# Performance work log

Hardware: AMD Instinct MI355X
Metric: run time of the kernel (lower is better)

Reference implementation:

```python
import jax, jax.numpy as jnp
import numpy as np

B, Hh, Ww, C, D = 32, 14, 14, 512, 8192

def setup_inputs() -> dict:
    key = jax.random.key(0)
    k1, k2, k3, k4, k5, k6 = jax.random.split(key, 6)
    bottom1 = jax.random.normal(k1, (B, Hh, Ww, C), dtype=jnp.float32)
    bottom2 = jax.random.normal(k2, (B, Hh, Ww, C), dtype=jnp.float32)
    # rand_s: random +/-1 (trainable weights in the original layer)
    rand_s_1 = (2.0 * jax.random.randint(k3, (C,), 0, 2).astype(jnp.float32) - 1.0)
    rand_s_2 = (2.0 * jax.random.randint(k4, (C,), 0, 2).astype(jnp.float32) - 1.0)
    # rand_h: hash bucket index in [0, D) per input channel (fixed, non-trainable)
    rand_h_1 = jax.random.randint(k5, (C,), 0, D, dtype=jnp.int32)
    rand_h_2 = jax.random.randint(k6, (C,), 0, D, dtype=jnp.int32)
    return {"bottom1": bottom1, "bottom2": bottom2,
            "rand_s_1": rand_s_1, "rand_s_2": rand_s_2,
            "rand_h_1": rand_h_1, "rand_h_2": rand_h_2}

def _count_sketch(x_flat, rand_s, rand_h, out_dim):
    # x_flat: [N, C]. Equivalent to x_flat @ sparse_sketch_matrix [C, out_dim]
    # where sketch[c, rand_h[c]] = rand_s[c].
    z = x_flat * rand_s                                   # [N, C]
    # scatter-add channels into their hash buckets along the feature axis
    return jax.ops.segment_sum(z.T, rand_h, num_segments=out_dim).T  # [N, D]

def reference(bottom1, bottom2, rand_s_1, rand_s_2, rand_h_1, rand_h_2):
    b, h, w, c1 = bottom1.shape
    c2 = bottom2.shape[-1]
    x1 = bottom1.reshape(-1, c1)
    x2 = bottom2.reshape(-1, c2)
    sk1 = _count_sketch(x1, rand_s_1, rand_h_1, D)        # [N, D]
    sk2 = _count_sketch(x2, rand_s_2, rand_h_2, D)        # [N, D]
    fft1 = jnp.fft.fft(sk1.astype(jnp.complex64), axis=-1)
    fft2 = jnp.fft.fft(sk2.astype(jnp.complex64), axis=-1)
    cbp_flat = jnp.real(jnp.fft.ifft(fft1 * fft2, axis=-1))  # circular conv
    cbp = cbp_flat.reshape(b, h, w, D)
    return jnp.sum(cbp, axis=(1, 2))                      # [B, D]
```

## Files before the change

kernel.cpp:

```cpp
#include <hip/hip_runtime.h>


#define NB   32
#define HW   196
#define CC   512
#define DD   8192
#define KP   224
#define NTHR 256
#define TILES_PER_B 16

typedef __attribute__((ext_vector_type(8)))  __bf16 bf8;
typedef __attribute__((ext_vector_type(16))) float  f32x16;

#define XT_ELEMS ((size_t)NB * CC * KP)
#define XT_BYTES (XT_ELEMS * 2)
#define PART_OFF_BYTES (2 * XT_BYTES)
#define PART_BYTES ((size_t)NB * TILES_PER_B * DD * 4)
#define NEED_FAST (PART_OFF_BYTES + PART_BYTES)
#define NEED_R5  PART_BYTES

__global__ __launch_bounds__(NTHR) void cbp_transpose_kernel(
    const float* __restrict__ x1, const float* __restrict__ x2,
    __bf16* __restrict__ xT1, __bf16* __restrict__ xT2)
{
    __shared__ float T[64][65];
    const int bid = blockIdx.x;
    const int b  = bid >> 5;
    const int ct = (bid >> 2) & 7;
    const int kt = bid & 3;
    const int tid = threadIdx.x;

    #pragma unroll
    for (int m = 0; m < 2; ++m) {
        const float* x   = m ? x2  : x1;
        __bf16*      xTo = m ? xT2 : xT1;

        #pragma unroll
        for (int p = 0; p < 4; ++p) {
            const int row  = p * 16 + (tid >> 4);
            const int col4 = (tid & 15) * 4;
            const int k = kt * 64 + row;
            float4 v = {0.f, 0.f, 0.f, 0.f};
            if (k < HW)
                v = *(const float4*)(x + ((size_t)(b * HW + k) * CC + ct * 64 + col4));
            T[col4 + 0][row] = v.x;
            T[col4 + 1][row] = v.y;
            T[col4 + 2][row] = v.z;
            T[col4 + 3][row] = v.w;
        }
        __syncthreads();

        const int c_l = tid >> 2;
        const int seg = tid & 3;
        const int kp0 = kt * 64 + seg * 16;
        if (kp0 < KP) {
            const size_t dstc = (size_t)(b * CC + ct * 64 + c_l) * KP;
            #pragma unroll
            for (int i2 = 0; i2 < 2; ++i2) {
                bf8 v;
                #pragma unroll
                for (int i = 0; i < 8; ++i)
                    v[i] = (__bf16)T[c_l][seg * 16 + i2 * 8 + i];
                *(bf8*)(xTo + dstc + kp0 + i2 * 8) = v;
            }
        }
        __syncthreads();
    }
}

__global__ __launch_bounds__(NTHR) void cbp_gram_t_kernel(
    const __bf16* __restrict__ xT1, const __bf16* __restrict__ xT2,
    const float* __restrict__ s1, const float* __restrict__ s2,
    const int*   __restrict__ h1, const int*   __restrict__ h2,
    float* __restrict__ partials)
{
    __shared__ float accD[DD];

    const int bid  = blockIdx.x;
    const int b    = bid >> 4;
    const int t1   = (bid >> 2) & 3;
    const int t2   = bid & 3;
    const int tid  = threadIdx.x;
    const int wid  = tid >> 6;
    const int lane = tid & 63;
    const int wr   = wid >> 1;
    const int wc   = wid & 1;
    const int lo5  = lane & 31;
    const int hi   = lane >> 5;

    for (int i = tid; i < DD; i += NTHR) accD[i] = 0.0f;
    __syncthreads();

    const int c1w = t1 * 128 + wr * 64;
    const int c2w = t2 * 128 + wc * 64;

    const __bf16* A0 = xT1 + ((size_t)(b * CC + c1w + lo5) * KP + hi * 8);
    const __bf16* A1 = A0 + (size_t)32 * KP;
    const __bf16* B0 = xT2 + ((size_t)(b * CC + c2w + lo5) * KP + hi * 8);
    const __bf16* B1 = B0 + (size_t)32 * KP;

    f32x16 acc00 = {}, acc01 = {}, acc10 = {}, acc11 = {};

    #pragma unroll
    for (int ks = 0; ks < KP / 16; ++ks) {
        const bf8 a0  = *(const bf8*)(A0 + ks * 16);
        const bf8 a1  = *(const bf8*)(A1 + ks * 16);
        const bf8 b0v = *(const bf8*)(B0 + ks * 16);
        const bf8 b1v = *(const bf8*)(B1 + ks * 16);
        acc00 = __builtin_amdgcn_mfma_f32_32x32x16_bf16(a0, b0v, acc00, 0, 0, 0);
        acc01 = __builtin_amdgcn_mfma_f32_32x32x16_bf16(a0, b1v, acc01, 0, 0, 0);
        acc10 = __builtin_amdgcn_mfma_f32_32x32x16_bf16(a1, b0v, acc10, 0, 0, 0);
        acc11 = __builtin_amdgcn_mfma_f32_32x32x16_bf16(a1, b1v, acc11, 0, 0, 0);
    }

    const float s2v0 = s2[c2w + lo5];
    const float s2v1 = s2[c2w + 32 + lo5];
    const int   h2v0 = h2[c2w + lo5];
    const int   h2v1 = h2[c2w + 32 + lo5];

    #pragma unroll
    for (int rt = 0; rt < 2; ++rt) {
        const f32x16 accL = rt ? acc10 : acc00;
        const f32x16 accR = rt ? acc11 : acc01;
        #pragma unroll
        for (int reg = 0; reg < 16; ++reg) {
            const int c1 = c1w + rt * 32 + (reg & 3) + 8 * (reg >> 2) + 4 * hi;
            const float sv = s1[c1];
            const int   hv = h1[c1];
            atomicAdd(&accD[(hv + h2v0) & (DD - 1)], sv * s2v0 * accL[reg]);
            atomicAdd(&accD[(hv + h2v1) & (DD - 1)], sv * s2v1 * accR[reg]);
        }
    }
    __syncthreads();

    float4* dst = (float4*)(partials + (size_t)bid * DD);
    const float4* src = (const float4*)accD;
    #pragma unroll
    for (int i = 0; i < DD / 4 / NTHR; ++i)
        dst[tid + i * NTHR] = src[tid + i * NTHR];
}

__global__ __launch_bounds__(NTHR) void cbp_mfma_kernel(
    const float* __restrict__ x1, const float* __restrict__ x2,
    const float* __restrict__ s1, const float* __restrict__ s2,
    const int*   __restrict__ h1, const int*   __restrict__ h2,
    float* __restrict__ ws, float* __restrict__ out, int use_ws)
{
    __shared__ float accD[DD];
    const int bid  = blockIdx.x;
    const int b    = bid >> 4;
    const int t1   = (bid >> 2) & 3;
    const int t2   = bid & 3;
    const int tid  = threadIdx.x;
    const int wid  = tid >> 6;
    const int lane = tid & 63;
    const int wr   = wid >> 1;
    const int wc   = wid & 1;
    const int lo5  = lane & 31;
    const int hi   = lane >> 5;

    for (int i = tid; i < DD; i += NTHR) accD[i] = 0.0f;
    __syncthreads();

    const int c1w = t1 * 128 + wr * 64;
    const int c2w = t2 * 128 + wc * 64;
    const float* A0 = x1 + (size_t)b * HW * CC + (c1w + lo5);
    const float* A1 = A0 + 32;
    const float* B0 = x2 + (size_t)b * HW * CC + (c2w + lo5);
    const float* B1 = B0 + 32;

    f32x16 acc00 = {}, acc01 = {}, acc10 = {}, acc11 = {};
    for (int ks = 0; ks < 12; ++ks) {
        const int kb = ks * 16 + hi * 8;
        bf8 a0, a1, b0v, b1v;
        #pragma unroll
        for (int j = 0; j < 8; ++j) {
            const size_t off = (size_t)(kb + j) * CC;
            a0[j] = (__bf16)A0[off]; a1[j] = (__bf16)A1[off];
            b0v[j] = (__bf16)B0[off]; b1v[j] = (__bf16)B1[off];
        }
        acc00 = __builtin_amdgcn_mfma_f32_32x32x16_bf16(a0, b0v, acc00, 0, 0, 0);
        acc01 = __builtin_amdgcn_mfma_f32_32x32x16_bf16(a0, b1v, acc01, 0, 0, 0);
        acc10 = __builtin_amdgcn_mfma_f32_32x32x16_bf16(a1, b0v, acc10, 0, 0, 0);
        acc11 = __builtin_amdgcn_mfma_f32_32x32x16_bf16(a1, b1v, acc11, 0, 0, 0);
    }
    {
        const int kb = 192 + hi * 8;
        bf8 a0, a1, b0v, b1v;
        #pragma unroll
        for (int j = 0; j < 8; ++j) {
            const int k = kb + j;
            const size_t off = (size_t)k * CC;
            const bool v = (k < HW);
            a0[j]  = (__bf16)(v ? A0[off] : 0.0f);
            a1[j]  = (__bf16)(v ? A1[off] : 0.0f);
            b0v[j] = (__bf16)(v ? B0[off] : 0.0f);
            b1v[j] = (__bf16)(v ? B1[off] : 0.0f);
        }
        acc00 = __builtin_amdgcn_mfma_f32_32x32x16_bf16(a0, b0v, acc00, 0, 0, 0);
        acc01 = __builtin_amdgcn_mfma_f32_32x32x16_bf16(a0, b1v, acc01, 0, 0, 0);
        acc10 = __builtin_amdgcn_mfma_f32_32x32x16_bf16(a1, b0v, acc10, 0, 0, 0);
        acc11 = __builtin_amdgcn_mfma_f32_32x32x16_bf16(a1, b1v, acc11, 0, 0, 0);
    }

    const float s2v0 = s2[c2w + lo5];
    const float s2v1 = s2[c2w + 32 + lo5];
    const int   h2v0 = h2[c2w + lo5];
    const int   h2v1 = h2[c2w + 32 + lo5];
    #pragma unroll
    for (int rt = 0; rt < 2; ++rt) {
        const f32x16 accL = rt ? acc10 : acc00;
        const f32x16 accR = rt ? acc11 : acc01;
        #pragma unroll
        for (int reg = 0; reg < 16; ++reg) {
            const int c1 = c1w + rt * 32 + (reg & 3) + 8 * (reg >> 2) + 4 * hi;
            const float sv = s1[c1];
            const int   hv = h1[c1];
            atomicAdd(&accD[(hv + h2v0) & (DD - 1)], sv * s2v0 * accL[reg]);
            atomicAdd(&accD[(hv + h2v1) & (DD - 1)], sv * s2v1 * accR[reg]);
        }
    }
    __syncthreads();

    if (use_ws) {
        float4* dst = (float4*)(ws + (size_t)bid * DD);
        const float4* src = (const float4*)accD;
        #pragma unroll
        for (int i = 0; i < DD / 4 / NTHR; ++i)
            dst[tid + i * NTHR] = src[tid + i * NTHR];
    } else {
        float* ob = out + (size_t)b * DD;
        for (int i = tid; i < DD; i += NTHR)
            atomicAdd(&ob[i], accD[i]);
    }
}

__global__ __launch_bounds__(NTHR) void cbp_reduce_kernel(
    const float* __restrict__ parts, float* __restrict__ out)
{
    const int b  = blockIdx.x >> 3;
    const int d0 = (blockIdx.x & 7) * 1024 + threadIdx.x * 4;
    const float* base = parts + (size_t)b * TILES_PER_B * DD + d0;
    float4 sum = {0.f, 0.f, 0.f, 0.f};
    #pragma unroll
    for (int t = 0; t < TILES_PER_B; ++t) {
        float4 v = *(const float4*)(base + (size_t)t * DD);
        sum.x += v.x; sum.y += v.y; sum.z += v.z; sum.w += v.w;
    }
    *(float4*)(out + (size_t)b * DD + d0) = sum;
}

extern "C" void kernel_launch(void* const* d_in, const int* in_sizes, int n_in,
                              void* d_out, int out_size, void* d_ws, size_t ws_size,
                              hipStream_t stream) {
    const float* x1 = (const float*)d_in[0];
    const float* x2 = (const float*)d_in[1];
    const float* s1 = (const float*)d_in[2];
    const float* s2 = (const float*)d_in[3];
    const int*   h1 = (const int*)d_in[4];
    const int*   h2 = (const int*)d_in[5];
    float* out = (float*)d_out;

    dim3 block(NTHR);
    if (ws_size >= NEED_FAST) {
        __bf16* xT1 = (__bf16*)d_ws;
        __bf16* xT2 = xT1 + XT_ELEMS;
        float*  parts = (float*)((char*)d_ws + PART_OFF_BYTES);
        cbp_transpose_kernel<<<dim3(NB * 32), block, 0, stream>>>(x1, x2, xT1, xT2);
        cbp_gram_t_kernel<<<dim3(NB * TILES_PER_B), block, 0, stream>>>(
            xT1, xT2, s1, s2, h1, h2, parts);
        cbp_reduce_kernel<<<dim3(NB * 8), block, 0, stream>>>(parts, out);
    } else if (ws_size >= NEED_R5) {
        float* parts = (float*)d_ws;
        cbp_mfma_kernel<<<dim3(NB * TILES_PER_B), block, 0, stream>>>(
            x1, x2, s1, s2, h1, h2, parts, out, 1);
        cbp_reduce_kernel<<<dim3(NB * 8), block, 0, stream>>>(parts, out);
    } else {
        hipMemsetAsync(out, 0, (size_t)out_size * sizeof(float), stream);
        cbp_mfma_kernel<<<dim3(NB * TILES_PER_B), block, 0, stream>>>(
            x1, x2, s1, s2, h1, h2, (float*)d_ws, out, 0);
    }
}
```

Measured before the change: 143.1 us.

## Split gram and hash-scatter into separate kernels, drop transpose pass

```diff
diff --git a/kernel.cpp b/kernel.cpp
--- a/kernel.cpp
+++ b/kernel.cpp
@@ -5,77 +5,22 @@
 #define HW   196
 #define CC   512
 #define DD   8192
-#define KP   224
 #define NTHR 256
 #define TILES_PER_B 16
 
 typedef __attribute__((ext_vector_type(8)))  __bf16 bf8;
 typedef __attribute__((ext_vector_type(16))) float  f32x16;
 
-#define XT_ELEMS ((size_t)NB * CC * KP)
-#define XT_BYTES (XT_ELEMS * 2)
-#define PART_OFF_BYTES (2 * XT_BYTES)
+#define G_BYTES   ((size_t)NB * TILES_PER_B * 128 * 128 * 4)
 #define PART_BYTES ((size_t)NB * TILES_PER_B * DD * 4)
-#define NEED_FAST (PART_OFF_BYTES + PART_BYTES)
-#define NEED_R5  PART_BYTES
-
-__global__ __launch_bounds__(NTHR) void cbp_transpose_kernel(
+#define NEED_SPLIT (G_BYTES + PART_BYTES)
+#define NEED_R5   PART_BYTES
+
+__global__ __launch_bounds__(NTHR) void cbp_gram_store_kernel(
     const float* __restrict__ x1, const float* __restrict__ x2,
-    __bf16* __restrict__ xT1, __bf16* __restrict__ xT2)
-{
-    __shared__ float T[64][65];
-    const int bid = blockIdx.x;
-    const int b  = bid >> 5;
-    const int ct = (bid >> 2) & 7;
-    const int kt = bid & 3;
-    const int tid = threadIdx.x;
-
-    #pragma unroll
-    for (int m = 0; m < 2; ++m) {
-        const float* x   = m ? x2  : x1;
-        __bf16*      xTo = m ? xT2 : xT1;
-
-        #pragma unroll
-        for (int p = 0; p < 4; ++p) {
-            const int row  = p * 16 + (tid >> 4);
-            const int col4 = (tid & 15) * 4;
-            const int k = kt * 64 + row;
-            float4 v = {0.f, 0.f, 0.f, 0.f};
-            if (k < HW)
-                v = *(const float4*)(x + ((size_t)(b * HW + k) * CC + ct * 64 + col4));
-            T[col4 + 0][row] = v.x;
-            T[col4 + 1][row] = v.y;
-            T[col4 + 2][row] = v.z;
-            T[col4 + 3][row] = v.w;
-        }
-        __syncthreads();
-
-        const int c_l = tid >> 2;
-        const int seg = tid & 3;
-        const int kp0 = kt * 64 + seg * 16;
-        if (kp0 < KP) {
-            const size_t dstc = (size_t)(b * CC + ct * 64 + c_l) * KP;
-            #pragma unroll
-            for (int i2 = 0; i2 < 2; ++i2) {
-                bf8 v;
-                #pragma unroll
-                for (int i = 0; i < 8; ++i)
-                    v[i] = (__bf16)T[c_l][seg * 16 + i2 * 8 + i];
-                *(bf8*)(xTo + dstc + kp0 + i2 * 8) = v;
-            }
-        }
-        __syncthreads();
-    }
-}
-
-__global__ __launch_bounds__(NTHR) void cbp_gram_t_kernel(
-    const __bf16* __restrict__ xT1, const __bf16* __restrict__ xT2,
     const float* __restrict__ s1, const float* __restrict__ s2,
-    const int*   __restrict__ h1, const int*   __restrict__ h2,
-    float* __restrict__ partials)
-{
-    __shared__ float accD[DD];
-
+    float* __restrict__ G)
+{
     const int bid  = blockIdx.x;
     const int b    = bid >> 4;
     const int t1   = (bid >> 2) & 3;
@@ -88,48 +33,99 @@
     const int lo5  = lane & 31;
     const int hi   = lane >> 5;
 
-    for (int i = tid; i < DD; i += NTHR) accD[i] = 0.0f;
-    __syncthreads();
-
     const int c1w = t1 * 128 + wr * 64;
     const int c2w = t2 * 128 + wc * 64;
 
-    const __bf16* A0 = xT1 + ((size_t)(b * CC + c1w + lo5) * KP + hi * 8);
-    const __bf16* A1 = A0 + (size_t)32 * KP;
-    const __bf16* B0 = xT2 + ((size_t)(b * CC + c2w + lo5) * KP + hi * 8);
-    const __bf16* B1 = B0 + (size_t)32 * KP;
+    const float* A0 = x1 + (size_t)b * HW * CC + (c1w + lo5);
+    const float* A1 = A0 + 32;
+    const float* B0 = x2 + (size_t)b * HW * CC + (c2w + lo5);
+    const float* B1 = B0 + 32;
+
+    const float sA0 = s1[c1w + lo5],      sA1 = s1[c1w + 32 + lo5];
+    const float sB0 = s2[c2w + lo5],      sB1 = s2[c2w + 32 + lo5];
 
     f32x16 acc00 = {}, acc01 = {}, acc10 = {}, acc11 = {};
 
-    #pragma unroll
-    for (int ks = 0; ks < KP / 16; ++ks) {
-        const bf8 a0  = *(const bf8*)(A0 + ks * 16);
-        const bf8 a1  = *(const bf8*)(A1 + ks * 16);
-        const bf8 b0v = *(const bf8*)(B0 + ks * 16);
-        const bf8 b1v = *(const bf8*)(B1 + ks * 16);
-        acc00 = __builtin_amdgcn_mfma_f32_32x32x16_bf16(a0, b0v, acc00, 0, 0, 0);
-        acc01 = __builtin_amdgcn_mfma_f32_32x32x16_bf16(a0, b1v, acc01, 0, 0, 0);
-        acc10 = __builtin_amdgcn_mfma_f32_32x32x16_bf16(a1, b0v, acc10, 0, 0, 0);
-        acc11 = __builtin_amdgcn_mfma_f32_32x32x16_bf16(a1, b1v, acc11, 0, 0, 0);
-    }
-
-    const float s2v0 = s2[c2w + lo5];
-    const float s2v1 = s2[c2w + 32 + lo5];
-    const int   h2v0 = h2[c2w + lo5];
-    const int   h2v1 = h2[c2w + 32 + lo5];
-
+    for (int ks = 0; ks < 12; ++ks) {
+        const int kb = ks * 16 + hi * 8;
+        bf8 a0, a1, b0v, b1v;
+        #pragma unroll
+        for (int j = 0; j < 8; ++j) {
+            const size_t off = (size_t)(kb + j) * CC;
+            a0[j]  = (__bf16)(A0[off] * sA0);
+            a1[j]  = (__bf16)(A1[off] * sA1);
+            b0v[j] = (__bf16)(B0[off] * sB0);
+            b1v[j] = (__bf16)(B1[off] * sB1);
+        }
+        acc00 = __builtin_amdgcn_mfma_f32_32x32x16_bf16(a0, b0v, acc00, 0, 0, 0);
+        acc01 = __builtin_amdgcn_mfma_f32_32x32x16_bf16(a0, b1v, acc01, 0, 0, 0);
+        acc10 = __builtin_amdgcn_mfma_f32_32x32x16_bf16(a1, b0v, acc10, 0, 0, 0);
+        acc11 = __builtin_amdgcn_mfma_f32_32x32x16_bf16(a1, b1v, acc11, 0, 0, 0);
+    }
+    {
+        const int kb = 192 + hi * 8;
+        bf8 a0, a1, b0v, b1v;
+        #pragma unroll
+        for (int j = 0; j < 8; ++j) {
+            const int k = kb + j;
+            const size_t off = (size_t)k * CC;
+            const bool v = (k < HW);
+            a0[j]  = (__bf16)(v ? A0[off] * sA0 : 0.0f);
+            a1[j]  = (__bf16)(v ? A1[off] * sA1 : 0.0f);
+            b0v[j] = (__bf16)(v ? B0[off] * sB0 : 0.0f);
+            b1v[j] = (__bf16)(v ? B1[off] * sB1 : 0.0f);
+        }
+        acc00 = __builtin_amdgcn_mfma_f32_32x32x16_bf16(a0, b0v, acc00, 0, 0, 0);
+        acc01 = __builtin_amdgcn_mfma_f32_32x32x16_bf16(a0, b1v, acc01, 0, 0, 0);
+        acc10 = __builtin_amdgcn_mfma_f32_32x32x16_bf16(a1, b0v, acc10, 0, 0, 0);
+        acc11 = __builtin_amdgcn_mfma_f32_32x32x16_bf16(a1, b1v, acc11, 0, 0, 0);
+    }
+
+    float* Gt = G + (size_t)bid * (128 * 128);
     #pragma unroll
     for (int rt = 0; rt < 2; ++rt) {
         const f32x16 accL = rt ? acc10 : acc00;
         const f32x16 accR = rt ? acc11 : acc01;
         #pragma unroll
         for (int reg = 0; reg < 16; ++reg) {
-            const int c1 = c1w + rt * 32 + (reg & 3) + 8 * (reg >> 2) + 4 * hi;
-            const float sv = s1[c1];
-            const int   hv = h1[c1];
-            atomicAdd(&accD[(hv + h2v0) & (DD - 1)], sv * s2v0 * accL[reg]);
-            atomicAdd(&accD[(hv + h2v1) & (DD - 1)], sv * s2v1 * accR[reg]);
-        }
+            const int c1l = wr * 64 + rt * 32 + (reg & 3) + 8 * (reg >> 2) + 4 * hi;
+            Gt[c1l * 128 + wc * 64 + lo5]      = accL[reg];
+            Gt[c1l * 128 + wc * 64 + 32 + lo5] = accR[reg];
+        }
+    }
+}
+
+__global__ __launch_bounds__(NTHR) void cbp_scatter_kernel(
+    const float* __restrict__ G,
+    const int* __restrict__ h1, const int* __restrict__ h2,
+    float* __restrict__ partials)
+{
+    __shared__ float accD[DD];
+    __shared__ int   h1t[128];
+    __shared__ int   h2t[128];
+
+    const int bid = blockIdx.x;
+    const int t1  = (bid >> 2) & 3;
+    const int t2  = bid & 3;
+    const int tid = threadIdx.x;
+
+    if (tid < 128)      h1t[tid]       = h1[t1 * 128 + tid];
+    else if (tid < 256) h2t[tid - 128] = h2[t2 * 128 + (tid - 128)];
+    for (int i = tid; i < DD; i += NTHR) accD[i] = 0.0f;
+    __syncthreads();
+
+    const float4* Gt = (const float4*)(G + (size_t)bid * (128 * 128));
+    #pragma unroll
+    for (int i = 0; i < 16; ++i) {
+        const int idx  = tid + i * NTHR;
+        const int c1l  = idx >> 5;
+        const int c2l4 = (idx & 31) * 4;
+        const float4 v = Gt[idx];
+        const int hb = h1t[c1l];
+        unsafeAtomicAdd(&accD[(hb + h2t[c2l4 + 0]) & (DD - 1)], v.x);
+        unsafeAtomicAdd(&accD[(hb + h2t[c2l4 + 1]) & (DD - 1)], v.y);
+        unsafeAtomicAdd(&accD[(hb + h2t[c2l4 + 2]) & (DD - 1)], v.z);
+        unsafeAtomicAdd(&accD[(hb + h2t[c2l4 + 3]) & (DD - 1)], v.w);
     }
     __syncthreads();
 
@@ -138,6 +134,21 @@
     #pragma unroll
     for (int i = 0; i < DD / 4 / NTHR; ++i)
         dst[tid + i * NTHR] = src[tid + i * NTHR];
+}
+
+__global__ __launch_bounds__(NTHR) void cbp_reduce_kernel(
+    const float* __restrict__ parts, float* __restrict__ out)
+{
+    const int b  = blockIdx.x >> 3;
+    const int d0 = (blockIdx.x & 7) * 1024 + threadIdx.x * 4;
+    const float* base = parts + (size_t)b * TILES_PER_B * DD + d0;
+    float4 sum = {0.f, 0.f, 0.f, 0.f};
+    #pragma unroll
+    for (int t = 0; t < TILES_PER_B; ++t) {
+        float4 v = *(const float4*)(base + (size_t)t * DD);
+        sum.x += v.x; sum.y += v.y; sum.z += v.z; sum.w += v.w;
+    }
+    *(float4*)(out + (size_t)b * DD + d0) = sum;
 }
 
 __global__ __launch_bounds__(NTHR) void cbp_mfma_kernel(
@@ -216,8 +227,8 @@
             const int c1 = c1w + rt * 32 + (reg & 3) + 8 * (reg >> 2) + 4 * hi;
             const float sv = s1[c1];
             const int   hv = h1[c1];
-            atomicAdd(&accD[(hv + h2v0) & (DD - 1)], sv * s2v0 * accL[reg]);
-            atomicAdd(&accD[(hv + h2v1) & (DD - 1)], sv * s2v1 * accR[reg]);
+            unsafeAtomicAdd(&accD[(hv + h2v0) & (DD - 1)], sv * s2v0 * accL[reg]);
+            unsafeAtomicAdd(&accD[(hv + h2v1) & (DD - 1)], sv * s2v1 * accR[reg]);
         }
     }
     __syncthreads();
@@ -233,21 +244,6 @@
         for (int i = tid; i < DD; i += NTHR)
             atomicAdd(&ob[i], accD[i]);
     }
-}
-
-__global__ __launch_bounds__(NTHR) void cbp_reduce_kernel(
-    const float* __restrict__ parts, float* __restrict__ out)
-{
-    const int b  = blockIdx.x >> 3;
-    const int d0 = (blockIdx.x & 7) * 1024 + threadIdx.x * 4;
-    const float* base = parts + (size_t)b * TILES_PER_B * DD + d0;
-    float4 sum = {0.f, 0.f, 0.f, 0.f};
-    #pragma unroll
-    for (int t = 0; t < TILES_PER_B; ++t) {
-        float4 v = *(const float4*)(base + (size_t)t * DD);
-        sum.x += v.x; sum.y += v.y; sum.z += v.z; sum.w += v.w;
-    }
-    *(float4*)(out + (size_t)b * DD + d0) = sum;
 }
 
 extern "C" void kernel_launch(void* const* d_in, const int* in_sizes, int n_in,
@@ -262,13 +258,13 @@
     float* out = (float*)d_out;
 
     dim3 block(NTHR);
-    if (ws_size >= NEED_FAST) {
-        __bf16* xT1 = (__bf16*)d_ws;
-        __bf16* xT2 = xT1 + XT_ELEMS;
-        float*  parts = (float*)((char*)d_ws + PART_OFF_BYTES);
-        cbp_transpose_kernel<<<dim3(NB * 32), block, 0, stream>>>(x1, x2, xT1, xT2);
-        cbp_gram_t_kernel<<<dim3(NB * TILES_PER_B), block, 0, stream>>>(
-            xT1, xT2, s1, s2, h1, h2, parts);
+    if (ws_size >= NEED_SPLIT) {
+        float* G     = (float*)d_ws;
+        float* parts = (float*)((char*)d_ws + G_BYTES);
+        cbp_gram_store_kernel<<<dim3(NB * TILES_PER_B), block, 0, stream>>>(
+            x1, x2, s1, s2, G);
+        cbp_scatter_kernel<<<dim3(NB * TILES_PER_B), block, 0, stream>>>(
+            G, h1, h2, parts);
         cbp_reduce_kernel<<<dim3(NB * 8), block, 0, stream>>>(parts, out);
     } else if (ws_size >= NEED_R5) {
         float* parts = (float*)d_ws;
```

Measured after the change: 178.7 us. 1.25x slower.

## Split Gram GEMM from hash scatter into separate kernels with sign folding

Applied to the files above, without the earlier changes.

```diff
diff --git a/kernel.cpp b/kernel.cpp
--- a/kernel.cpp
+++ b/kernel.cpp
@@ -12,15 +12,16 @@
 typedef __attribute__((ext_vector_type(8)))  __bf16 bf8;
 typedef __attribute__((ext_vector_type(16))) float  f32x16;
 
-#define XT_ELEMS ((size_t)NB * CC * KP)
-#define XT_BYTES (XT_ELEMS * 2)
-#define PART_OFF_BYTES (2 * XT_BYTES)
+#define G_BYTES    ((size_t)NB * TILES_PER_B * 128 * 128 * 4)
+#define XT_ELEMS   ((size_t)NB * CC * KP)
+#define XT_BYTES   (XT_ELEMS * 2)
 #define PART_BYTES ((size_t)NB * TILES_PER_B * DD * 4)
-#define NEED_FAST (PART_OFF_BYTES + PART_BYTES)
-#define NEED_R5  PART_BYTES
+#define NEED_SPLIT (G_BYTES + PART_BYTES)
+#define NEED_R5    PART_BYTES
 
 __global__ __launch_bounds__(NTHR) void cbp_transpose_kernel(
     const float* __restrict__ x1, const float* __restrict__ x2,
+    const float* __restrict__ s1, const float* __restrict__ s2,
     __bf16* __restrict__ xT1, __bf16* __restrict__ xT2)
 {
     __shared__ float T[64][65];
@@ -33,6 +34,7 @@
     #pragma unroll
     for (int m = 0; m < 2; ++m) {
         const float* x   = m ? x2  : x1;
+        const float* s   = m ? s2  : s1;
         __bf16*      xTo = m ? xT2 : xT1;
 
         #pragma unroll
@@ -54,13 +56,14 @@
         const int seg = tid & 3;
         const int kp0 = kt * 64 + seg * 16;
         if (kp0 < KP) {
+            const float sv = s[ct * 64 + c_l];
             const size_t dstc = (size_t)(b * CC + ct * 64 + c_l) * KP;
             #pragma unroll
             for (int i2 = 0; i2 < 2; ++i2) {
                 bf8 v;
                 #pragma unroll
                 for (int i = 0; i < 8; ++i)
-                    v[i] = (__bf16)T[c_l][seg * 16 + i2 * 8 + i];
+                    v[i] = (__bf16)(T[c_l][seg * 16 + i2 * 8 + i] * sv);
                 *(bf8*)(xTo + dstc + kp0 + i2 * 8) = v;
             }
         }
@@ -68,68 +71,88 @@
     }
 }
 
-__global__ __launch_bounds__(NTHR) void cbp_gram_t_kernel(
+__global__ __launch_bounds__(NTHR, 5) void cbp_gram2_kernel(
     const __bf16* __restrict__ xT1, const __bf16* __restrict__ xT2,
-    const float* __restrict__ s1, const float* __restrict__ s2,
-    const int*   __restrict__ h1, const int*   __restrict__ h2,
-    float* __restrict__ partials)
-{
-    __shared__ float accD[DD];
-
+    float* __restrict__ G)
+{
     const int bid  = blockIdx.x;
-    const int b    = bid >> 4;
-    const int t1   = (bid >> 2) & 3;
-    const int t2   = bid & 3;
+    const int swz  = (bid & 7) * 256 + (bid >> 3);
     const int tid  = threadIdx.x;
     const int wid  = tid >> 6;
     const int lane = tid & 63;
-    const int wr   = wid >> 1;
-    const int wc   = wid & 1;
     const int lo5  = lane & 31;
     const int hi   = lane >> 5;
 
+    const int t  = swz * 4 + wid;
+    const int b  = t >> 8;
+    const int r  = t & 255;
+    const int u1 = r >> 4;
+    const int u2 = r & 15;
+
+    const __bf16* A  = xT1 + ((size_t)(b * CC + u1 * 32 + lo5) * KP + hi * 8);
+    const __bf16* Bp = xT2 + ((size_t)(b * CC + u2 * 32 + lo5) * KP + hi * 8);
+
+    f32x16 acc = {};
+    bf8 Af[7], Bf[7];
+
+    #pragma unroll
+    for (int s = 0; s < 7; ++s) {
+        Af[s] = *(const bf8*)(A  + s * 16);
+        Bf[s] = *(const bf8*)(Bp + s * 16);
+    }
+    #pragma unroll
+    for (int s = 0; s < 7; ++s)
+        acc = __builtin_amdgcn_mfma_f32_32x32x16_bf16(Af[s], Bf[s], acc, 0, 0, 0);
+
+    #pragma unroll
+    for (int s = 0; s < 7; ++s) {
+        Af[s] = *(const bf8*)(A  + (7 + s) * 16);
+        Bf[s] = *(const bf8*)(Bp + (7 + s) * 16);
+    }
+    #pragma unroll
+    for (int s = 0; s < 7; ++s)
+        acc = __builtin_amdgcn_mfma_f32_32x32x16_bf16(Af[s], Bf[s], acc, 0, 0, 0);
+
+    float* Gt = G + (size_t)(b * 16 + (u1 >> 2) * 4 + (u2 >> 2)) * (128 * 128);
+    const int c2l = (u2 & 3) * 32 + lo5;
+    #pragma unroll
+    for (int reg = 0; reg < 16; ++reg) {
+        const int c1l = (u1 & 3) * 32 + (reg & 3) + 8 * (reg >> 2) + 4 * hi;
+        Gt[c1l * 128 + c2l] = acc[reg];
+    }
+}
+
+__global__ __launch_bounds__(NTHR) void cbp_scatter_kernel(
+    const float* __restrict__ G,
+    const int* __restrict__ h1, const int* __restrict__ h2,
+    float* __restrict__ partials)
+{
+    __shared__ float accD[DD];
+    __shared__ int   h1t[128];
+    __shared__ int   h2t[128];
+
+    const int bid = blockIdx.x;
+    const int t1  = (bid >> 2) & 3;
+    const int t2  = bid & 3;
+    const int tid = threadIdx.x;
+
+    if (tid < 128)      h1t[tid]       = h1[t1 * 128 + tid];
+    else if (tid < 256) h2t[tid - 128] = h2[t2 * 128 + (tid - 128)];
     for (int i = tid; i < DD; i += NTHR) accD[i] = 0.0f;
     __syncthreads();
 
-    const int c1w = t1 * 128 + wr * 64;
-    const int c2w = t2 * 128 + wc * 64;
-
-    const __bf16* A0 = xT1 + ((size_t)(b * CC + c1w + lo5) * KP + hi * 8);
-    const __bf16* A1 = A0 + (size_t)32 * KP;
-    const __bf16* B0 = xT2 + ((size_t)(b * CC + c2w + lo5) * KP + hi * 8);
-    const __bf16* B1 = B0 + (size_t)32 * KP;
-
-    f32x16 acc00 = {}, acc01 = {}, acc10 = {}, acc11 = {};
-
-    #pragma unroll
-    for (int ks = 0; ks < KP / 16; ++ks) {
-        const bf8 a0  = *(const bf8*)(A0 + ks * 16);
-        const bf8 a1  = *(const bf8*)(A1 + ks * 16);
-        const bf8 b0v = *(const bf8*)(B0 + ks * 16);
-        const bf8 b1v = *(const bf8*)(B1 + ks * 16);
-        acc00 = __builtin_amdgcn_mfma_f32_32x32x16_bf16(a0, b0v, acc00, 0, 0, 0);
-        acc01 = __builtin_amdgcn_mfma_f32_32x32x16_bf16(a0, b1v, acc01, 0, 0, 0);
-        acc10 = __builtin_amdgcn_mfma_f32_32x32x16_bf16(a1, b0v, acc10, 0, 0, 0);
-        acc11 = __builtin_amdgcn_mfma_f32_32x32x16_bf16(a1, b1v, acc11, 0, 0, 0);
-    }
-
-    const float s2v0 = s2[c2w + lo5];
-    const float s2v1 = s2[c2w + 32 + lo5];
-    const int   h2v0 = h2[c2w + lo5];
-    const int   h2v1 = h2[c2w + 32 + lo5];
-
-    #pragma unroll
-    for (int rt = 0; rt < 2; ++rt) {
-        const f32x16 accL = rt ? acc10 : acc00;
-        const f32x16 accR = rt ? acc11 : acc01;
-        #pragma unroll
-        for (int reg = 0; reg < 16; ++reg) {
-            const int c1 = c1w + rt * 32 + (reg & 3) + 8 * (reg >> 2) + 4 * hi;
-            const float sv = s1[c1];
-            const int   hv = h1[c1];
-            atomicAdd(&accD[(hv + h2v0) & (DD - 1)], sv * s2v0 * accL[reg]);
-            atomicAdd(&accD[(hv + h2v1) & (DD - 1)], sv * s2v1 * accR[reg]);
-        }
+    const float4* Gt = (const float4*)(G + (size_t)bid * (128 * 128));
+    #pragma unroll
+    for (int i = 0; i < 16; ++i) {
+        const int idx  = tid + i * NTHR;
+        const int c1l  = idx >> 5;
+        const int c2l4 = (idx & 31) * 4;
+        const float4 v = Gt[idx];
+        const int hb = h1t[c1l];
+        unsafeAtomicAdd(&accD[(hb + h2t[c2l4 + 0]) & (DD - 1)], v.x);
+        unsafeAtomicAdd(&accD[(hb + h2t[c2l4 + 1]) & (DD - 1)], v.y);
+        unsafeAtomicAdd(&accD[(hb + h2t[c2l4 + 2]) & (DD - 1)], v.z);
+        unsafeAtomicAdd(&accD[(hb + h2t[c2l4 + 3]) & (DD - 1)], v.w);
     }
     __syncthreads();
 
@@ -138,6 +161,21 @@
     #pragma unroll
     for (int i = 0; i < DD / 4 / NTHR; ++i)
         dst[tid + i * NTHR] = src[tid + i * NTHR];
+}
+
+__global__ __launch_bounds__(NTHR) void cbp_reduce_kernel(
+    const float* __restrict__ parts, float* __restrict__ out)
+{
+    const int b  = blockIdx.x >> 3;
+    const int d0 = (blockIdx.x & 7) * 1024 + threadIdx.x * 4;
+    const float* base = parts + (size_t)b * TILES_PER_B * DD + d0;
+    float4 sum = {0.f, 0.f, 0.f, 0.f};
+    #pragma unroll
+    for (int t = 0; t < TILES_PER_B; ++t) {
+        float4 v = *(const float4*)(base + (size_t)t * DD);
+        sum.x += v.x; sum.y += v.y; sum.z += v.z; sum.w += v.w;
+    }
+    *(float4*)(out + (size_t)b * DD + d0) = sum;
 }
 
 __global__ __launch_bounds__(NTHR) void cbp_mfma_kernel(
@@ -216,8 +254,8 @@
             const int c1 = c1w + rt * 32 + (reg & 3) + 8 * (reg >> 2) + 4 * hi;
             const float sv = s1[c1];
             const int   hv = h1[c1];
-            atomicAdd(&accD[(hv + h2v0) & (DD - 1)], sv * s2v0 * accL[reg]);
-            atomicAdd(&accD[(hv + h2v1) & (DD - 1)], sv * s2v1 * accR[reg]);
+            unsafeAtomicAdd(&accD[(hv + h2v0) & (DD - 1)], sv * s2v0 * accL[reg]);
+            unsafeAtomicAdd(&accD[(hv + h2v1) & (DD - 1)], sv * s2v1 * accR[reg]);
         }
     }
     __syncthreads();
@@ -233,21 +271,6 @@
         for (int i = tid; i < DD; i += NTHR)
             atomicAdd(&ob[i], accD[i]);
     }
-}
-
-__global__ __launch_bounds__(NTHR) void cbp_reduce_kernel(
-    const float* __restrict__ parts, float* __restrict__ out)
-{
-    const int b  = blockIdx.x >> 3;
-    const int d0 = (blockIdx.x & 7) * 1024 + threadIdx.x * 4;
-    const float* base = parts + (size_t)b * TILES_PER_B * DD + d0;
-    float4 sum = {0.f, 0.f, 0.f, 0.f};
-    #pragma unroll
-    for (int t = 0; t < TILES_PER_B; ++t) {
-        float4 v = *(const float4*)(base + (size_t)t * DD);
-        sum.x += v.x; sum.y += v.y; sum.z += v.z; sum.w += v.w;
-    }
-    *(float4*)(out + (size_t)b * DD + d0) = sum;
 }
 
 extern "C" void kernel_launch(void* const* d_in, const int* in_sizes, int n_in,
@@ -262,13 +285,16 @@
     float* out = (float*)d_out;
 
     dim3 block(NTHR);
-    if (ws_size >= NEED_FAST) {
-        __bf16* xT1 = (__bf16*)d_ws;
-        __bf16* xT2 = xT1 + XT_ELEMS;
-        float*  parts = (float*)((char*)d_ws + PART_OFF_BYTES);
-        cbp_transpose_kernel<<<dim3(NB * 32), block, 0, stream>>>(x1, x2, xT1, xT2);
-        cbp_gram_t_kernel<<<dim3(NB * TILES_PER_B), block, 0, stream>>>(
-            xT1, xT2, s1, s2, h1, h2, parts);
+    if (ws_size >= NEED_SPLIT) {
+        float*  G     = (float*)d_ws;
+        __bf16* xT1   = (__bf16*)((char*)d_ws + G_BYTES);
+        __bf16* xT2   = xT1 + XT_ELEMS;
+        float*  parts = (float*)((char*)d_ws + G_BYTES);
+        cbp_transpose_kernel<<<dim3(NB * 32), block, 0, stream>>>(
+            x1, x2, s1, s2, xT1, xT2);
+        cbp_gram2_kernel<<<dim3(2048), block, 0, stream>>>(xT1, xT2, G);
+        cbp_scatter_kernel<<<dim3(NB * TILES_PER_B), block, 0, stream>>>(
+            G, h1, h2, parts);
         cbp_reduce_kernel<<<dim3(NB * 8), block, 0, stream>>>(parts, out);
     } else if (ws_size >= NEED_R5) {
         float* parts = (float*)d_ws;
```

Measured after the change: 150.9 us. 1.05x slower.

## Fold sign vectors into transpose, cache hashes in LDS, batch MFMA loads

Applied to the files above, without the earlier changes.

```diff
diff --git a/kernel.cpp b/kernel.cpp
--- a/kernel.cpp
+++ b/kernel.cpp
@@ -12,15 +12,15 @@
 typedef __attribute__((ext_vector_type(8)))  __bf16 bf8;
 typedef __attribute__((ext_vector_type(16))) float  f32x16;
 
-#define XT_ELEMS ((size_t)NB * CC * KP)
-#define XT_BYTES (XT_ELEMS * 2)
-#define PART_OFF_BYTES (2 * XT_BYTES)
+#define XT_ELEMS   ((size_t)NB * CC * KP)
+#define XT_BYTES   (XT_ELEMS * 2)
 #define PART_BYTES ((size_t)NB * TILES_PER_B * DD * 4)
-#define NEED_FAST (PART_OFF_BYTES + PART_BYTES)
-#define NEED_R5  PART_BYTES
+#define NEED_FUSED (2 * XT_BYTES + PART_BYTES)
+#define NEED_R5    PART_BYTES
 
 __global__ __launch_bounds__(NTHR) void cbp_transpose_kernel(
     const float* __restrict__ x1, const float* __restrict__ x2,
+    const float* __restrict__ s1, const float* __restrict__ s2,
     __bf16* __restrict__ xT1, __bf16* __restrict__ xT2)
 {
     __shared__ float T[64][65];
@@ -33,6 +33,7 @@
     #pragma unroll
     for (int m = 0; m < 2; ++m) {
         const float* x   = m ? x2  : x1;
+        const float* s   = m ? s2  : s1;
         __bf16*      xTo = m ? xT2 : xT1;
 
         #pragma unroll
@@ -54,13 +55,14 @@
         const int seg = tid & 3;
         const int kp0 = kt * 64 + seg * 16;
         if (kp0 < KP) {
+            const float sv = s[ct * 64 + c_l];
             const size_t dstc = (size_t)(b * CC + ct * 64 + c_l) * KP;
             #pragma unroll
             for (int i2 = 0; i2 < 2; ++i2) {
                 bf8 v;
                 #pragma unroll
                 for (int i = 0; i < 8; ++i)
-                    v[i] = (__bf16)T[c_l][seg * 16 + i2 * 8 + i];
+                    v[i] = (__bf16)(T[c_l][seg * 16 + i2 * 8 + i] * sv);
                 *(bf8*)(xTo + dstc + kp0 + i2 * 8) = v;
             }
         }
@@ -68,15 +70,17 @@
     }
 }
 
-__global__ __launch_bounds__(NTHR) void cbp_gram_t_kernel(
+__global__ __launch_bounds__(NTHR, 2) void cbp_gram_scatter_kernel(
     const __bf16* __restrict__ xT1, const __bf16* __restrict__ xT2,
-    const float* __restrict__ s1, const float* __restrict__ s2,
-    const int*   __restrict__ h1, const int*   __restrict__ h2,
+    const int* __restrict__ h1, const int* __restrict__ h2,
     float* __restrict__ partials)
 {
     __shared__ float accD[DD];
-
-    const int bid  = blockIdx.x;
+    __shared__ int   h1t[128];
+    __shared__ int   h2t[128];
+
+    const int bid0 = blockIdx.x;
+    const int bid  = (bid0 & 7) * 64 + (bid0 >> 3);
     const int b    = bid >> 4;
     const int t1   = (bid >> 2) & 3;
     const int t2   = bid & 3;
@@ -88,47 +92,51 @@
     const int lo5  = lane & 31;
     const int hi   = lane >> 5;
 
+    if (tid < 128)      h1t[tid]       = h1[t1 * 128 + tid];
+    else if (tid < 256) h2t[tid - 128] = h2[t2 * 128 + (tid - 128)];
     for (int i = tid; i < DD; i += NTHR) accD[i] = 0.0f;
-    __syncthreads();
-
-    const int c1w = t1 * 128 + wr * 64;
-    const int c2w = t2 * 128 + wc * 64;
-
-    const __bf16* A0 = xT1 + ((size_t)(b * CC + c1w + lo5) * KP + hi * 8);
+
+    const __bf16* A0 = xT1 + ((size_t)(b * CC + t1 * 128 + wr * 64 + lo5) * KP + hi * 8);
     const __bf16* A1 = A0 + (size_t)32 * KP;
-    const __bf16* B0 = xT2 + ((size_t)(b * CC + c2w + lo5) * KP + hi * 8);
+    const __bf16* B0 = xT2 + ((size_t)(b * CC + t2 * 128 + wc * 64 + lo5) * KP + hi * 8);
     const __bf16* B1 = B0 + (size_t)32 * KP;
 
     f32x16 acc00 = {}, acc01 = {}, acc10 = {}, acc11 = {};
 
     #pragma unroll
-    for (int ks = 0; ks < KP / 16; ++ks) {
-        const bf8 a0  = *(const bf8*)(A0 + ks * 16);
-        const bf8 a1  = *(const bf8*)(A1 + ks * 16);
-        const bf8 b0v = *(const bf8*)(B0 + ks * 16);
-        const bf8 b1v = *(const bf8*)(B1 + ks * 16);
-        acc00 = __builtin_amdgcn_mfma_f32_32x32x16_bf16(a0, b0v, acc00, 0, 0, 0);
-        acc01 = __builtin_amdgcn_mfma_f32_32x32x16_bf16(a0, b1v, acc01, 0, 0, 0);
-        acc10 = __builtin_amdgcn_mfma_f32_32x32x16_bf16(a1, b0v, acc10, 0, 0, 0);
-        acc11 = __builtin_amdgcn_mfma_f32_32x32x16_bf16(a1, b1v, acc11, 0, 0, 0);
-    }
-
-    const float s2v0 = s2[c2w + lo5];
-    const float s2v1 = s2[c2w + 32 + lo5];
-    const int   h2v0 = h2[c2w + lo5];
-    const int   h2v1 = h2[c2w + 32 + lo5];
-
+    for (int half = 0; half < 2; ++half) {
+        const int kof = half * 7 * 16;
+        bf8 Af0[7], Af1[7], Bf0[7], Bf1[7];
+        #pragma unroll
+        for (int s = 0; s < 7; ++s) {
+            Af0[s] = *(const bf8*)(A0 + kof + s * 16);
+            Af1[s] = *(const bf8*)(A1 + kof + s * 16);
+            Bf0[s] = *(const bf8*)(B0 + kof + s * 16);
+            Bf1[s] = *(const bf8*)(B1 + kof + s * 16);
+        }
+        #pragma unroll
+        for (int s = 0; s < 7; ++s) {
+            acc00 = __builtin_amdgcn_mfma_f32_32x32x16_bf16(Af0[s], Bf0[s], acc00, 0, 0, 0);
+            acc01 = __builtin_amdgcn_mfma_f32_32x32x16_bf16(Af0[s], Bf1[s], acc01, 0, 0, 0);
+            acc10 = __builtin_amdgcn_mfma_f32_32x32x16_bf16(Af1[s], Bf0[s], acc10, 0, 0, 0);
+            acc11 = __builtin_amdgcn_mfma_f32_32x32x16_bf16(Af1[s], Bf1[s], acc11, 0, 0, 0);
+        }
+    }
+
+    __syncthreads();
+
+    const int h2v0 = h2t[wc * 64 + lo5];
+    const int h2v1 = h2t[wc * 64 + 32 + lo5];
     #pragma unroll
     for (int rt = 0; rt < 2; ++rt) {
         const f32x16 accL = rt ? acc10 : acc00;
         const f32x16 accR = rt ? acc11 : acc01;
         #pragma unroll
         for (int reg = 0; reg < 16; ++reg) {
-            const int c1 = c1w + rt * 32 + (reg & 3) + 8 * (reg >> 2) + 4 * hi;
-            const float sv = s1[c1];
-            const int   hv = h1[c1];
-            atomicAdd(&accD[(hv + h2v0) & (DD - 1)], sv * s2v0 * accL[reg]);
-            atomicAdd(&accD[(hv + h2v1) & (DD - 1)], sv * s2v1 * accR[reg]);
+            const int c1l = wr * 64 + rt * 32 + (reg & 3) + 8 * (reg >> 2) + 4 * hi;
+            const int hb  = h1t[c1l];
+            unsafeAtomicAdd(&accD[(hb + h2v0) & (DD - 1)], accL[reg]);
+            unsafeAtomicAdd(&accD[(hb + h2v1) & (DD - 1)], accR[reg]);
         }
     }
     __syncthreads();
@@ -138,6 +146,21 @@
     #pragma unroll
     for (int i = 0; i < DD / 4 / NTHR; ++i)
         dst[tid + i * NTHR] = src[tid + i * NTHR];
+}
+
+__global__ __launch_bounds__(NTHR) void cbp_reduce_kernel(
+    const float* __restrict__ parts, float* __restrict__ out)
+{
+    const int b  = blockIdx.x >> 3;
+    const int d0 = (blockIdx.x & 7) * 1024 + threadIdx.x * 4;
+    const float* base = parts + (size_t)b * TILES_PER_B * DD + d0;
+    float4 sum = {0.f, 0.f, 0.f, 0.f};
+    #pragma unroll
+    for (int t = 0; t < TILES_PER_B; ++t) {
+        float4 v = *(const float4*)(base + (size_t)t * DD);
+        sum.x += v.x; sum.y += v.y; sum.z += v.z; sum.w += v.w;
+    }
+    *(float4*)(out + (size_t)b * DD + d0) = sum;
 }
 
 __global__ __launch_bounds__(NTHR) void cbp_mfma_kernel(
@@ -216,8 +239,8 @@
             const int c1 = c1w + rt * 32 + (reg & 3) + 8 * (reg >> 2) + 4 * hi;
             const float sv = s1[c1];
             const int   hv = h1[c1];
-            atomicAdd(&accD[(hv + h2v0) & (DD - 1)], sv * s2v0 * accL[reg]);
-            atomicAdd(&accD[(hv + h2v1) & (DD - 1)], sv * s2v1 * accR[reg]);
+            unsafeAtomicAdd(&accD[(hv + h2v0) & (DD - 1)], sv * s2v0 * accL[reg]);
+            unsafeAtomicAdd(&accD[(hv + h2v1) & (DD - 1)], sv * s2v1 * accR[reg]);
         }
     }
     __syncthreads();
@@ -233,21 +256,6 @@
         for (int i = tid; i < DD; i += NTHR)
             atomicAdd(&ob[i], accD[i]);
     }
-}
-
-__global__ __launch_bounds__(NTHR) void cbp_reduce_kernel(
-    const float* __restrict__ parts, float* __restrict__ out)
-{
-    const int b  = blockIdx.x >> 3;
-    const int d0 = (blockIdx.x & 7) * 1024 + threadIdx.x * 4;
-    const float* base = parts + (size_t)b * TILES_PER_B * DD + d0;
-    float4 sum = {0.f, 0.f, 0.f, 0.f};
-    #pragma unroll
-    for (int t = 0; t < TILES_PER_B; ++t) {
-        float4 v = *(const float4*)(base + (size_t)t * DD);
-        sum.x += v.x; sum.y += v.y; sum.z += v.z; sum.w += v.w;
-    }
-    *(float4*)(out + (size_t)b * DD + d0) = sum;
 }
 
 extern "C" void kernel_launch(void* const* d_in, const int* in_sizes, int n_in,
@@ -262,13 +270,14 @@
     float* out = (float*)d_out;
 
     dim3 block(NTHR);
-    if (ws_size >= NEED_FAST) {
-        __bf16* xT1 = (__bf16*)d_ws;
-        __bf16* xT2 = xT1 + XT_ELEMS;
-        float*  parts = (float*)((char*)d_ws + PART_OFF_BYTES);
-        cbp_transpose_kernel<<<dim3(NB * 32), block, 0, stream>>>(x1, x2, xT1, xT2);
-        cbp_gram_t_kernel<<<dim3(NB * TILES_PER_B), block, 0, stream>>>(
-            xT1, xT2, s1, s2, h1, h2, parts);
+    if (ws_size >= NEED_FUSED) {
+        __bf16* xT1   = (__bf16*)d_ws;
+        __bf16* xT2   = xT1 + XT_ELEMS;
+        float*  parts = (float*)((char*)d_ws + 2 * XT_BYTES);
+        cbp_transpose_kernel<<<dim3(NB * 32), block, 0, stream>>>(
+            x1, x2, s1, s2, xT1, xT2);
+        cbp_gram_scatter_kernel<<<dim3(NB * TILES_PER_B), block, 0, stream>>>(
+            xT1, xT2, h1, h2, parts);
         cbp_reduce_kernel<<<dim3(NB * 8), block, 0, stream>>>(parts, out);
     } else if (ws_size >= NEED_R5) {
         float* parts = (float*)d_ws;
```

Measured after the change: 141.2 us. Within noise of the previous version (-1.3%).
